# Performance work log

Measured on AMD Instinct MI355X. Metric: run time of the kernel, lower is better.

The kernel has to match this reference:

```python
import jax, jax.numpy as jnp
import numpy as np

F, K, V, ITERS = 150000, 5, 100000, 5
S = 2 ** K  # factor state space
MLP_SIZE = 2 * ITERS * S + ITERS * 2  # 330
NEG = -1e30
SHIFT = -500.0

# static bit table: bits[state, slot] in {0,1}
_BITS = ((np.arange(S)[:, None] >> np.arange(K)[None, :]) & 1).astype(np.int32)  # [S,K]
_BITS_T = jnp.asarray(_BITS.T)  # [K,S]
# mask bias for grouped logsumexp: bias[slot, b, state] = 0 if bits[state,slot]==b else NEG
_BIAS = jnp.asarray(np.where(_BITS.T[:, None, :] == np.arange(2)[None, :, None], 0.0, NEG).astype(np.float32))  # [K,2,S]


def neg_inf_to_zero(x):
    return jnp.where(jnp.isneginf(x), 0.0, x)


def expand(msg):
    # msg [F,K,2] -> [F,K,S]: broadcast each slot message over factor states by that slot's bit
    return msg[:, jnp.arange(K)[:, None], _BITS_T]


def setup_inputs() -> dict:
    key = jax.random.key(0)
    k0, k1 = jax.random.split(key)
    factor_potentials = jax.random.normal(k0, (F, S), dtype=jnp.float32)
    var_idx = jax.random.randint(k1, (F, K), 0, V, dtype=jnp.int32)
    prv_v2f = jnp.zeros((F, K, 2), jnp.float32)
    prv_f2v = jnp.zeros((F, K, 2), jnp.float32)
    prv_fb = jax.nn.log_softmax(factor_potentials, axis=1)
    # bethe MLP initialized exactly as in the torch module
    lin1_w = jnp.eye(MLP_SIZE, dtype=jnp.float32)
    lin1_b = jnp.zeros((MLP_SIZE,), jnp.float32)
    num_ones = 2 * S + 2
    lin2_w = jnp.zeros((1, MLP_SIZE), jnp.float32).at[0, -num_ones:].set(1.0)
    lin2_b = jnp.zeros((1,), jnp.float32)
    return {"factor_potentials": factor_potentials, "var_idx": var_idx,
            "prv_v2f": prv_v2f, "prv_f2v": prv_f2v, "prv_fb": prv_fb,
            "lin1_w": lin1_w, "lin1_b": lin1_b, "lin2_w": lin2_w, "lin2_b": lin2_b}


def _shifted_relu(x):
    return jnp.maximum(x, SHIFT)


def reference(factor_potentials, var_idx, prv_v2f, prv_f2v, prv_fb, lin1_w, lin1_b, lin2_w, lin2_b):
    var_flat = var_idx.reshape(-1)
    deg = jax.ops.segment_sum(jnp.ones((F * K,), jnp.float32), var_flat, num_segments=V)  # var_degrees
    pooled_states = []
    fb, v2f = prv_fb, prv_v2f
    for _ in range(ITERS):
        # factor->var messages, no double counting: subtract the slot's own incoming message
        scores = fb[:, None, :] - expand(v2f)                    # [F,K,S]
        m = jax.nn.logsumexp(scores[:, :, None, :] + _BIAS[None], axis=-1)  # [F,K,2]
        m = jax.nn.log_softmax(m, axis=-1)
        # var beliefs: gather all incoming factor->var messages
        vb = jax.ops.segment_sum(m.reshape(-1, 2), var_flat, num_segments=V)  # [V,2]
        vb = jax.nn.log_softmax(vb, axis=-1)
        # var->factor messages, no double counting
        v2f = jax.nn.log_softmax(vb[var_idx] - m, axis=-1)        # [F,K,2]
        # factor beliefs
        fb = factor_potentials + expand(v2f).sum(axis=1)          # [F,S]
        fb = fb - jax.nn.logsumexp(fb, axis=1, keepdims=True)
        # pooled Bethe free-energy features for this iteration
        e_fb = jnp.exp(fb)
        energy = jnp.sum(e_fb * neg_inf_to_zero(factor_potentials), axis=0)     # [S]
        fac_ent = -jnp.sum(e_fb * neg_inf_to_zero(fb), axis=0)                  # [S]
        var_term = jnp.sum((deg - 1.0)[:, None] * jnp.exp(vb) * neg_inf_to_zero(vb), axis=0)  # [2]
        pooled_states.append(jnp.concatenate([energy, fac_ent, var_term])[None, :])  # [1, 2S+2]
    x = jnp.concatenate(pooled_states, axis=1)   # [1, MLP_SIZE]
    h = _shifted_relu(x @ lin1_w.T + lin1_b)
    out = _shifted_relu(h @ lin2_w.T + lin2_b)   # [1,1] estimated ln(Z)
    return out
```

## Files before the change

### kernel.cpp

```cpp
#include <hip/hip_runtime.h>

#define F_N   150000
#define K_N   5
#define S_N   32
#define V_N   100000
#define NITER 5
#define MLP_N 330
#define SHIFTV (-500.0f)
#define W_ELL 32
#define DEG_PAD 16

#define FBLK  ((F_N + 255) / 256)
#define GBLK  ((V_N * 8 + 255) / 256)
#define EBLK  ((F_N * K_N + 255) / 256)
#define BBLK  (6 * FBLK)

__device__ __forceinline__ float lse2(float a, float b) {
    float mx = fmaxf(a, b);
    return mx + __logf(__expf(a - mx) + __expf(b - mx));
}

__global__ __launch_bounds__(256) void k_build(
    const float* __restrict__ prv_fb,
    const float* __restrict__ prv_v2f,
    const int*   __restrict__ vidx,
    float2*      __restrict__ m_out,
    int*         __restrict__ deg,
    int*         __restrict__ ellpos)
{
    int g = blockIdx.x / 6, r = blockIdx.x % 6;

    if (r < 5) {
        int e = (g * 5 + r) * 256 + threadIdx.x;
        if (e >= F_N * K_N) return;
        int v = vidx[e];
        int pos = atomicAdd(&deg[v * DEG_PAD], 1);
        ellpos[e] = (pos < W_ELL) ? v * W_ELL + pos : V_N * W_ELL;
        return;
    }

    int f = g * 256 + threadIdx.x;
    if (f >= F_N) return;

    float fb[S_N];
    const float4* p4 = reinterpret_cast<const float4*>(prv_fb + (size_t)f * S_N);
    #pragma unroll
    for (int i = 0; i < S_N / 4; ++i) {
        float4 v = p4[i];
        fb[i*4+0] = v.x; fb[i*4+1] = v.y; fb[i*4+2] = v.z; fb[i*4+3] = v.w;
    }
    float M = fb[0];
    #pragma unroll
    for (int s = 1; s < S_N; ++s) M = fmaxf(M, fb[s]);
    float T = 0.0f;
    float S0[K_N] = {0.f, 0.f, 0.f, 0.f, 0.f};
    #pragma unroll
    for (int s = 0; s < S_N; ++s) {
        float t = __expf(fb[s] - M);
        T += t;
        #pragma unroll
        for (int k = 0; k < K_N; ++k)
            if (((s >> k) & 1) == 0) S0[k] += t;
    }
    #pragma unroll
    for (int k = 0; k < K_N; ++k) {
        float v0 = prv_v2f[(size_t)f * (K_N*2) + k*2 + 0];
        float v1 = prv_v2f[(size_t)f * (K_N*2) + k*2 + 1];
        float u0 = __logf(S0[k])     - v0;
        float u1 = __logf(T - S0[k]) - v1;
        float l  = lse2(u0, u1);
        m_out[k*F_N + f] = make_float2(u0 - l, u1 - l);
    }
}

__global__ __launch_bounds__(256) void k_scatter0(
    const int*    __restrict__ ellpos,
    const float2* __restrict__ m,
    float2*       __restrict__ mell)
{
    int e = blockIdx.x * 256 + threadIdx.x;
    if (e >= F_N * K_N) return;
    int f = e / K_N;
    int k = e - f * K_N;
    mell[ellpos[e]] = m[k * F_N + f];
}

__global__ __launch_bounds__(256) void k_gather(
    const float2* __restrict__ mell,
    const int*    __restrict__ deg,
    float2*       __restrict__ vb,
    float2*       __restrict__ cpart,
    int iter)
{
    __shared__ float2 wred[4];
    int t = blockIdx.x * 256 + threadIdx.x;
    int v = t >> 3, sub = t & 7;
    int lane = threadIdx.x & 63;

    float a0 = 0.0f, a1 = 0.0f;
    int n = 0;
    if (v < V_N) {
        n = deg[v * DEG_PAD];
        int nn = n < W_ELL ? n : W_ELL;
        const float2* row = mell + (size_t)v * W_ELL;
        for (int i = sub; i < nn; i += 8) {
            float2 mm = row[i];
            a0 += mm.x; a1 += mm.y;
        }
    }
    a0 += __shfl_xor(a0, 1); a1 += __shfl_xor(a1, 1);
    a0 += __shfl_xor(a0, 2); a1 += __shfl_xor(a1, 2);
    a0 += __shfl_xor(a0, 4); a1 += __shfl_xor(a1, 4);

    float c0 = 0.0f, c1 = 0.0f;
    if (v < V_N && sub == 0) {
        vb[v] = make_float2(a0, a1);
        float l = lse2(a0, a1);
        float b0 = a0 - l, b1 = a1 - l;
        float dm1 = (float)n - 1.0f;
        c0 = dm1 * __expf(b0) * b0;
        c1 = dm1 * __expf(b1) * b1;
    }
    #pragma unroll
    for (int mk = 32; mk >= 1; mk >>= 1) {
        c0 += __shfl_xor(c0, mk);
        c1 += __shfl_xor(c1, mk);
    }
    if (lane == 0) wred[threadIdx.x >> 6] = make_float2(c0, c1);
    __syncthreads();
    if (threadIdx.x == 0) {
        float2 s = wred[0];
        s.x += wred[1].x + wred[2].x + wred[3].x;
        s.y += wred[1].y + wred[2].y + wred[3].y;
        cpart[iter * GBLK + blockIdx.x] = s;
    }
}

template <bool LAST>
__global__ __launch_bounds__(256) void k_iter(
    const float*  __restrict__ pot,
    const int*    __restrict__ vidx,
    const int*    __restrict__ ellpos,
    float2*       __restrict__ m,
    float2*       __restrict__ mell,
    const float2* __restrict__ vb,
    float*        __restrict__ fpart,
    int iter)
{
    const int lane = threadIdx.x & 63;
    __shared__ float red[256];

    int f = blockIdx.x * 256 + threadIdx.x;
    bool valid = f < F_N;
    int fc = valid ? f : (F_N - 1);

    float2 mm[K_N];
    #pragma unroll
    for (int k = 0; k < K_N; ++k) mm[k] = m[k*F_N + fc];
    int vi[K_N];
    #pragma unroll
    for (int k = 0; k < K_N; ++k) vi[k] = vidx[(size_t)fc * K_N + k];

    float v2f[K_N][2];
    #pragma unroll
    for (int k = 0; k < K_N; ++k) {
        float2 b = vb[vi[k]];
        float a0 = b.x - mm[k].x;
        float a1 = b.y - mm[k].y;
        float l = lse2(a0, a1);
        v2f[k][0] = a0 - l;
        v2f[k][1] = a1 - l;
    }

    float fb[S_N];
    const float4* p4 = reinterpret_cast<const float4*>(pot + (size_t)fc * S_N);
    #pragma unroll
    for (int i = 0; i < S_N / 4; ++i) {
        float4 pv = p4[i];
        int s = i * 4;
        fb[s+0] = pv.x + v2f[0][(s+0)&1] + v2f[1][((s+0)>>1)&1] + v2f[2][((s+0)>>2)&1] + v2f[3][((s+0)>>3)&1] + v2f[4][((s+0)>>4)&1];
        fb[s+1] = pv.y + v2f[0][(s+1)&1] + v2f[1][((s+1)>>1)&1] + v2f[2][((s+1)>>2)&1] + v2f[3][((s+1)>>3)&1] + v2f[4][((s+1)>>4)&1];
        fb[s+2] = pv.z + v2f[0][(s+2)&1] + v2f[1][((s+2)>>1)&1] + v2f[2][((s+2)>>2)&1] + v2f[3][((s+2)>>3)&1] + v2f[4][((s+2)>>4)&1];
        fb[s+3] = pv.w + v2f[0][(s+3)&1] + v2f[1][((s+3)>>1)&1] + v2f[2][((s+3)>>2)&1] + v2f[3][((s+3)>>3)&1] + v2f[4][((s+3)>>4)&1];
    }

    float M = fb[0];
    #pragma unroll
    for (int s = 1; s < S_N; ++s) M = fmaxf(M, fb[s]);

    float T = 0.0f;
    float S0[K_N] = {0.f, 0.f, 0.f, 0.f, 0.f};
    #pragma unroll
    for (int s = 0; s < S_N; ++s) {
        float t = __expf(fb[s] - M);
        T += t;
        #pragma unroll
        for (int k = 0; k < K_N; ++k)
            if (((s >> k) & 1) == 0) S0[k] += t;
    }

    if (!LAST) {
        int el[K_N];
        #pragma unroll
        for (int k = 0; k < K_N; ++k) el[k] = ellpos[(size_t)fc * K_N + k];
        #pragma unroll
        for (int k = 0; k < K_N; ++k) {
            float u0 = __logf(S0[k])     - v2f[k][0];
            float u1 = __logf(T - S0[k]) - v2f[k][1];
            float l  = lse2(u0, u1);
            if (valid) {
                float2 nm = make_float2(u0 - l, u1 - l);
                m[k*F_N + f] = nm;
                mell[el[k]]  = nm;
            }
        }
    }

    float invT = 1.0f / T;
    float logT = __logf(T);
    float arr[2 * S_N];
    #pragma unroll
    for (int s = 0; s < S_N; ++s) {
        float p   = __expf(fb[s] - M) * invT;
        float fbn = fb[s] - M - logT;
        float w   = v2f[0][s&1] + v2f[1][(s>>1)&1] + v2f[2][(s>>2)&1]
                  + v2f[3][(s>>3)&1] + v2f[4][(s>>4)&1];
        float po  = fb[s] - w;
        arr[s]       = valid ? p * po   : 0.0f;
        arr[S_N + s] = valid ? -p * fbn : 0.0f;
    }

    #pragma unroll
    for (int mk = 32; mk >= 1; mk >>= 1) {
        bool upper = (lane & mk) != 0;
        #pragma unroll
        for (int j = 0; j < mk; ++j) {
            float send = upper ? arr[j] : arr[j + mk];
            float recv = __shfl_xor(send, mk);
            float keep = upper ? arr[j + mk] : arr[j];
            arr[j] = keep + recv;
        }
    }

    red[threadIdx.x] = arr[0];
    __syncthreads();
    if (threadIdx.x < 64) {
        float s = red[threadIdx.x] + red[64 + threadIdx.x]
                + red[128 + threadIdx.x] + red[192 + threadIdx.x];
        fpart[((size_t)iter * FBLK + blockIdx.x) * 64 + threadIdx.x] = s;
    }
}

__global__ __launch_bounds__(256) void k_vt(
    const float*  __restrict__ fpart,
    const float2* __restrict__ cpart,
    float*        __restrict__ x)
{
    __shared__ float red[256];
    int b = blockIdx.x, t = threadIdx.x;
    float acc = 0.0f;
    if (b < 320) {
        int it = b >> 6, s = b & 63;
        for (int i = t; i < FBLK; i += 256)
            acc += fpart[((size_t)it * FBLK + i) * 64 + s];
    } else {
        int idx = b - 320;
        int it = idx >> 1, c = idx & 1;
        for (int i = t; i < GBLK; i += 256) {
            float2 p = cpart[it * GBLK + i];
            acc += c ? p.y : p.x;
        }
    }
    red[t] = acc;
    __syncthreads();
    #pragma unroll
    for (int off = 128; off >= 1; off >>= 1) {
        if (t < off) red[t] += red[t + off];
        __syncthreads();
    }
    if (t == 0) {
        if (b < 320) {
            int it = b >> 6, s = b & 63;
            x[it*66 + s] = red[0];
        } else {
            int idx = b - 320;
            int it = idx >> 1, c = idx & 1;
            x[it*66 + 64 + c] = red[0];
        }
    }
}

__global__ __launch_bounds__(64) void k_mlp1(
    const float* __restrict__ x, const float* __restrict__ w1,
    const float* __restrict__ b1, float* __restrict__ h)
{
    int j = blockIdx.x;
    int lane = threadIdx.x;
    float s = 0.0f;
    for (int i = lane; i < MLP_N; i += 64) s += x[i] * w1[(size_t)j * MLP_N + i];
    #pragma unroll
    for (int mk = 32; mk >= 1; mk >>= 1) s += __shfl_xor(s, mk);
    if (lane == 0) h[j] = fmaxf(s + b1[j], SHIFTV);
}

__global__ __launch_bounds__(64) void k_mlp2(
    const float* __restrict__ h, const float* __restrict__ w2,
    const float* __restrict__ b2, float* __restrict__ out)
{
    int lane = threadIdx.x;
    float s = 0.0f;
    for (int i = lane; i < MLP_N; i += 64) s += h[i] * w2[i];
    #pragma unroll
    for (int mk = 32; mk >= 1; mk >>= 1) s += __shfl_xor(s, mk);
    if (lane == 0) out[0] = fmaxf(s + b2[0], SHIFTV);
}

extern "C" void kernel_launch(void* const* d_in, const int* in_sizes, int n_in,
                              void* d_out, int out_size, void* d_ws, size_t ws_size,
                              hipStream_t stream)
{
    (void)in_sizes; (void)n_in; (void)out_size; (void)ws_size;
    const float* pot  = (const float*)d_in[0];
    const int*   vidx = (const int*)  d_in[1];
    const float* pv2f = (const float*)d_in[2];
    const float* pfb  = (const float*)d_in[4];
    const float* w1   = (const float*)d_in[5];
    const float* b1   = (const float*)d_in[6];
    const float* w2   = (const float*)d_in[7];
    const float* b2   = (const float*)d_in[8];

    float2* m      = (float2*)d_ws;
    float2* mell   = m + 5 * F_N;
    float2* vb     = mell + (size_t)V_N * W_ELL + 32;
    float2* cpart  = vb + V_N;
    float*  fpart  = (float*)(cpart + NITER * GBLK);
    float*  x      = fpart + (size_t)NITER * FBLK * 64;
    float*  h      = x + MLP_N;
    int*    ellpos = (int*)(h + MLP_N);
    int*    deg    = ellpos + (size_t)F_N * K_N;

    hipMemsetAsync(deg, 0, (size_t)V_N * DEG_PAD * sizeof(int), stream);

    k_build<<<BBLK, 256, 0, stream>>>(pfb, pv2f, vidx, m, deg, ellpos);
    k_scatter0<<<EBLK, 256, 0, stream>>>(ellpos, m, mell);

    for (int it = 0; it < NITER; ++it) {
        k_gather<<<GBLK, 256, 0, stream>>>(mell, deg, vb, cpart, it);
        if (it < NITER - 1)
            k_iter<false><<<FBLK, 256, 0, stream>>>(pot, vidx, ellpos, m, mell, vb, fpart, it);
        else
            k_iter<true><<<FBLK, 256, 0, stream>>>(pot, vidx, ellpos, m, mell, vb, fpart, it);
    }

    k_vt<<<330, 256, 0, stream>>>(fpart, cpart, x);
    k_mlp1<<<MLP_N, 64, 0, stream>>>(x, w1, b1, h);
    k_mlp2<<<1, 64, 0, stream>>>(h, w2, b2, (float*)d_out);
}
```

Measured before the change: 206.0 us.

## Split each factor across two threads, compact degree array, fuse MLP kernels

Each factor in k_iter is now handled by two lanes, each owning 16 of the 32 states. Max, sum and per-slot partials are combined with one shuffle, and the butterfly reduction starts at a 32-entry array with a remapped output index. The aim is to cut per-thread register pressure and serial work, raising occupancy. The change also compacts the padded degree array into a dense one for the gather kernel and fuses the two MLP kernels into a single block. The cost is duplicated v2f/gather work per factor, since both lanes compute it, and twice as many blocks and partial sums.

```diff
diff --git a/kernel.cpp b/kernel.cpp
--- a/kernel.cpp
+++ b/kernel.cpp
@@ -11,6 +11,7 @@
 #define DEG_PAD 16
 
 #define FBLK  ((F_N + 255) / 256)
+#define F2BLK ((2*F_N + 255) / 256)
 #define GBLK  ((V_N * 8 + 255) / 256)
 #define EBLK  ((F_N * K_N + 255) / 256)
 #define BBLK  (6 * FBLK)
@@ -76,9 +77,12 @@
 __global__ __launch_bounds__(256) void k_scatter0(
     const int*    __restrict__ ellpos,
     const float2* __restrict__ m,
-    float2*       __restrict__ mell)
+    const int*    __restrict__ deg,
+    float2*       __restrict__ mell,
+    int*          __restrict__ degc)
 {
     int e = blockIdx.x * 256 + threadIdx.x;
+    if (e < V_N) degc[e] = deg[e * DEG_PAD];
     if (e >= F_N * K_N) return;
     int f = e / K_N;
     int k = e - f * K_N;
@@ -87,7 +91,7 @@
 
 __global__ __launch_bounds__(256) void k_gather(
     const float2* __restrict__ mell,
-    const int*    __restrict__ deg,
+    const int*    __restrict__ degc,
     float2*       __restrict__ vb,
     float2*       __restrict__ cpart,
     int iter)
@@ -100,7 +104,7 @@
     float a0 = 0.0f, a1 = 0.0f;
     int n = 0;
     if (v < V_N) {
-        n = deg[v * DEG_PAD];
+        n = degc[v];
         int nn = n < W_ELL ? n : W_ELL;
         const float2* row = mell + (size_t)v * W_ELL;
         for (int i = sub; i < nn; i += 8) {
@@ -148,9 +152,10 @@
     int iter)
 {
     const int lane = threadIdx.x & 63;
-    __shared__ float red[256];
-
-    int f = blockIdx.x * 256 + threadIdx.x;
+    __shared__ float red[4][64];
+
+    int t = blockIdx.x * 256 + threadIdx.x;
+    int f = t >> 1, p = t & 1;
     bool valid = f < F_N;
     int fc = valid ? f : (F_N - 1);
 
@@ -172,82 +177,92 @@
         v2f[k][1] = a1 - l;
     }
 
-    float fb[S_N];
-    const float4* p4 = reinterpret_cast<const float4*>(pot + (size_t)fc * S_N);
-    #pragma unroll
-    for (int i = 0; i < S_N / 4; ++i) {
+    float fb[16];
+    const float4* p4 = reinterpret_cast<const float4*>(pot + (size_t)fc * S_N + p * 16);
+    #pragma unroll
+    for (int i = 0; i < 4; ++i) {
         float4 pv = p4[i];
-        int s = i * 4;
-        fb[s+0] = pv.x + v2f[0][(s+0)&1] + v2f[1][((s+0)>>1)&1] + v2f[2][((s+0)>>2)&1] + v2f[3][((s+0)>>3)&1] + v2f[4][((s+0)>>4)&1];
-        fb[s+1] = pv.y + v2f[0][(s+1)&1] + v2f[1][((s+1)>>1)&1] + v2f[2][((s+1)>>2)&1] + v2f[3][((s+1)>>3)&1] + v2f[4][((s+1)>>4)&1];
-        fb[s+2] = pv.z + v2f[0][(s+2)&1] + v2f[1][((s+2)>>1)&1] + v2f[2][((s+2)>>2)&1] + v2f[3][((s+2)>>3)&1] + v2f[4][((s+2)>>4)&1];
-        fb[s+3] = pv.w + v2f[0][(s+3)&1] + v2f[1][((s+3)>>1)&1] + v2f[2][((s+3)>>2)&1] + v2f[3][((s+3)>>3)&1] + v2f[4][((s+3)>>4)&1];
+        int s = p*16 + i*4;
+        fb[i*4+0] = pv.x + v2f[0][(s+0)&1] + v2f[1][((s+0)>>1)&1] + v2f[2][((s+0)>>2)&1] + v2f[3][((s+0)>>3)&1] + v2f[4][((s+0)>>4)&1];
+        fb[i*4+1] = pv.y + v2f[0][(s+1)&1] + v2f[1][((s+1)>>1)&1] + v2f[2][((s+1)>>2)&1] + v2f[3][((s+1)>>3)&1] + v2f[4][((s+1)>>4)&1];
+        fb[i*4+2] = pv.z + v2f[0][(s+2)&1] + v2f[1][((s+2)>>1)&1] + v2f[2][((s+2)>>2)&1] + v2f[3][((s+2)>>3)&1] + v2f[4][((s+2)>>4)&1];
+        fb[i*4+3] = pv.w + v2f[0][(s+3)&1] + v2f[1][((s+3)>>1)&1] + v2f[2][((s+3)>>2)&1] + v2f[3][((s+3)>>3)&1] + v2f[4][((s+3)>>4)&1];
     }
 
     float M = fb[0];
     #pragma unroll
-    for (int s = 1; s < S_N; ++s) M = fmaxf(M, fb[s]);
+    for (int j = 1; j < 16; ++j) M = fmaxf(M, fb[j]);
+    M = fmaxf(M, __shfl_xor(M, 1));
 
     float T = 0.0f;
     float S0[K_N] = {0.f, 0.f, 0.f, 0.f, 0.f};
     #pragma unroll
-    for (int s = 0; s < S_N; ++s) {
-        float t = __expf(fb[s] - M);
-        T += t;
+    for (int j = 0; j < 16; ++j) {
+        int s = p*16 + j;
+        float e = __expf(fb[j] - M);
+        T += e;
         #pragma unroll
         for (int k = 0; k < K_N; ++k)
-            if (((s >> k) & 1) == 0) S0[k] += t;
-    }
+            if (((s >> k) & 1) == 0) S0[k] += e;
+    }
+    T += __shfl_xor(T, 1);
+    #pragma unroll
+    for (int k = 0; k < K_N; ++k) S0[k] += __shfl_xor(S0[k], 1);
 
     if (!LAST) {
-        int el[K_N];
-        #pragma unroll
-        for (int k = 0; k < K_N; ++k) el[k] = ellpos[(size_t)fc * K_N + k];
         #pragma unroll
         for (int k = 0; k < K_N; ++k) {
-            float u0 = __logf(S0[k])     - v2f[k][0];
-            float u1 = __logf(T - S0[k]) - v2f[k][1];
-            float l  = lse2(u0, u1);
-            if (valid) {
+            bool mine = p ? (k >= 3) : (k < 3);
+            if (valid && mine) {
+                float u0 = __logf(S0[k])     - v2f[k][0];
+                float u1 = __logf(T - S0[k]) - v2f[k][1];
+                float l  = lse2(u0, u1);
                 float2 nm = make_float2(u0 - l, u1 - l);
                 m[k*F_N + f] = nm;
-                mell[el[k]]  = nm;
+                mell[ellpos[(size_t)f * K_N + k]] = nm;
             }
         }
     }
 
     float invT = 1.0f / T;
     float logT = __logf(T);
-    float arr[2 * S_N];
-    #pragma unroll
-    for (int s = 0; s < S_N; ++s) {
-        float p   = __expf(fb[s] - M) * invT;
-        float fbn = fb[s] - M - logT;
+    float arr[32];
+    #pragma unroll
+    for (int j = 0; j < 16; ++j) {
+        int s = p*16 + j;
+        float pe  = __expf(fb[j] - M) * invT;
+        float fbn = fb[j] - M - logT;
         float w   = v2f[0][s&1] + v2f[1][(s>>1)&1] + v2f[2][(s>>2)&1]
                   + v2f[3][(s>>3)&1] + v2f[4][(s>>4)&1];
-        float po  = fb[s] - w;
-        arr[s]       = valid ? p * po   : 0.0f;
-        arr[S_N + s] = valid ? -p * fbn : 0.0f;
-    }
-
-    #pragma unroll
-    for (int mk = 32; mk >= 1; mk >>= 1) {
+        arr[j]      = valid ? pe * (fb[j] - w) : 0.0f;
+        arr[16 + j] = valid ? -pe * fbn        : 0.0f;
+    }
+
+    int len = 16;
+    #pragma unroll
+    for (int mk = 2; mk <= 32; mk <<= 1) {
         bool upper = (lane & mk) != 0;
         #pragma unroll
-        for (int j = 0; j < mk; ++j) {
-            float send = upper ? arr[j] : arr[j + mk];
-            float recv = __shfl_xor(send, mk);
-            float keep = upper ? arr[j + mk] : arr[j];
-            arr[j] = keep + recv;
-        }
-    }
-
-    red[threadIdx.x] = arr[0];
+        for (int j = 0; j < 16; ++j) {
+            if (j < len) {
+                float send = upper ? arr[j] : arr[j + len];
+                float recv = __shfl_xor(send, mk);
+                float keep = upper ? arr[j + len] : arr[j];
+                arr[j] = keep + recv;
+            }
+        }
+        len >>= 1;
+    }
+    int jl = (((lane>>1)&1)<<4) | (((lane>>2)&1)<<3) | (((lane>>3)&1)<<2)
+           | (((lane>>4)&1)<<1) | ((lane>>5)&1);
+    int g  = (lane & 1) * 16 + jl + (jl < 16 ? 0 : 16);
+
+    red[threadIdx.x >> 6][g] = arr[0];
     __syncthreads();
     if (threadIdx.x < 64) {
-        float s = red[threadIdx.x] + red[64 + threadIdx.x]
-                + red[128 + threadIdx.x] + red[192 + threadIdx.x];
-        fpart[((size_t)iter * FBLK + blockIdx.x) * 64 + threadIdx.x] = s;
+        float s = red[0][threadIdx.x] + red[1][threadIdx.x]
+                + red[2][threadIdx.x] + red[3][threadIdx.x];
+        fpart[((size_t)iter * F2BLK + blockIdx.x) * 64 + threadIdx.x] = s;
     }
 }
 
@@ -261,8 +276,8 @@
     float acc = 0.0f;
     if (b < 320) {
         int it = b >> 6, s = b & 63;
-        for (int i = t; i < FBLK; i += 256)
-            acc += fpart[((size_t)it * FBLK + i) * 64 + s];
+        for (int i = t; i < F2BLK; i += 256)
+            acc += fpart[((size_t)it * F2BLK + i) * 64 + s];
     } else {
         int idx = b - 320;
         int it = idx >> 1, c = idx & 1;
@@ -290,29 +305,38 @@
     }
 }
 
-__global__ __launch_bounds__(64) void k_mlp1(
+__global__ __launch_bounds__(256) void k_mlp(
     const float* __restrict__ x, const float* __restrict__ w1,
-    const float* __restrict__ b1, float* __restrict__ h)
-{
-    int j = blockIdx.x;
-    int lane = threadIdx.x;
+    const float* __restrict__ b1, const float* __restrict__ w2,
+    const float* __restrict__ b2, float* __restrict__ out)
+{
+    __shared__ float xs[MLP_N];
+    __shared__ float hs[MLP_N];
+    __shared__ float red[256];
+    int t = threadIdx.x, wid = t >> 6, lane = t & 63;
+
+    for (int i = t; i < MLP_N; i += 256) xs[i] = x[i];
+    __syncthreads();
+
+    for (int j = wid; j < MLP_N; j += 4) {
+        float s = 0.0f;
+        for (int i = lane; i < MLP_N; i += 64) s += xs[i] * w1[(size_t)j * MLP_N + i];
+        #pragma unroll
+        for (int mk = 32; mk >= 1; mk >>= 1) s += __shfl_xor(s, mk);
+        if (lane == 0) hs[j] = fmaxf(s + b1[j], SHIFTV);
+    }
+    __syncthreads();
+
     float s = 0.0f;
-    for (int i = lane; i < MLP_N; i += 64) s += x[i] * w1[(size_t)j * MLP_N + i];
-    #pragma unroll
-    for (int mk = 32; mk >= 1; mk >>= 1) s += __shfl_xor(s, mk);
-    if (lane == 0) h[j] = fmaxf(s + b1[j], SHIFTV);
-}
-
-__global__ __launch_bounds__(64) void k_mlp2(
-    const float* __restrict__ h, const float* __restrict__ w2,
-    const float* __restrict__ b2, float* __restrict__ out)
-{
-    int lane = threadIdx.x;
-    float s = 0.0f;
-    for (int i = lane; i < MLP_N; i += 64) s += h[i] * w2[i];
-    #pragma unroll
-    for (int mk = 32; mk >= 1; mk >>= 1) s += __shfl_xor(s, mk);
-    if (lane == 0) out[0] = fmaxf(s + b2[0], SHIFTV);
+    for (int i = t; i < MLP_N; i += 256) s += hs[i] * w2[i];
+    red[t] = s;
+    __syncthreads();
+    #pragma unroll
+    for (int off = 128; off >= 1; off >>= 1) {
+        if (t < off) red[t] += red[t + off];
+        __syncthreads();
+    }
+    if (t == 0) out[0] = fmaxf(red[0] + b2[0], SHIFTV);
 }
 
 extern "C" void kernel_launch(void* const* d_in, const int* in_sizes, int n_in,
@@ -334,25 +358,24 @@
     float2* vb     = mell + (size_t)V_N * W_ELL + 32;
     float2* cpart  = vb + V_N;
     float*  fpart  = (float*)(cpart + NITER * GBLK);
-    float*  x      = fpart + (size_t)NITER * FBLK * 64;
-    float*  h      = x + MLP_N;
-    int*    ellpos = (int*)(h + MLP_N);
-    int*    deg    = ellpos + (size_t)F_N * K_N;
+    float*  x      = fpart + (size_t)NITER * F2BLK * 64;
+    int*    ellpos = (int*)(x + MLP_N);
+    int*    degc   = ellpos + (size_t)F_N * K_N;
+    int*    deg    = degc + V_N;
 
     hipMemsetAsync(deg, 0, (size_t)V_N * DEG_PAD * sizeof(int), stream);
 
     k_build<<<BBLK, 256, 0, stream>>>(pfb, pv2f, vidx, m, deg, ellpos);
-    k_scatter0<<<EBLK, 256, 0, stream>>>(ellpos, m, mell);
+    k_scatter0<<<EBLK, 256, 0, stream>>>(ellpos, m, deg, mell, degc);
 
     for (int it = 0; it < NITER; ++it) {
-        k_gather<<<GBLK, 256, 0, stream>>>(mell, deg, vb, cpart, it);
+        k_gather<<<GBLK, 256, 0, stream>>>(mell, degc, vb, cpart, it);
         if (it < NITER - 1)
-            k_iter<false><<<FBLK, 256, 0, stream>>>(pot, vidx, ellpos, m, mell, vb, fpart, it);
+            k_iter<false><<<F2BLK, 256, 0, stream>>>(pot, vidx, ellpos, m, mell, vb, fpart, it);
         else
-            k_iter<true><<<FBLK, 256, 0, stream>>>(pot, vidx, ellpos, m, mell, vb, fpart, it);
+            k_iter<true><<<F2BLK, 256, 0, stream>>>(pot, vidx, ellpos, m, mell, vb, fpart, it);
     }
 
     k_vt<<<330, 256, 0, stream>>>(fpart, cpart, x);
-    k_mlp1<<<MLP_N, 64, 0, stream>>>(x, w1, b1, h);
-    k_mlp2<<<1, 64, 0, stream>>>(h, w2, b2, (float*)d_out);
-}
+    k_mlp<<<1, 256, 0, stream>>>(x, w1, b1, w2, b2, (float*)d_out);
+}
```

After: 461.9 us. 124% more time.

## Fuse initial message build with ELL scatter, one thread per edge

Applied to the files above, without the earlier changes.

Merges the initial factor-to-variable message computation and the ELL scatter into one kernel with one thread per (factor, slot) edge. Each thread does its degree atomic, computes its own slot message and writes it straight into the ELL buffer, which removes the separate scatter launch and the reread of m. The degree array is now unpadded, so the memset is smaller and the gather reads degrees contiguously, but atomics on neighbouring counters may contend more. In exchange, each of the 5 slot threads reloads and re-exponentiates the same 32-float factor belief row, so that exp work is done five times over.

```diff
diff --git a/kernel.cpp b/kernel.cpp
--- a/kernel.cpp
+++ b/kernel.cpp
@@ -8,12 +8,10 @@
 #define MLP_N 330
 #define SHIFTV (-500.0f)
 #define W_ELL 32
-#define DEG_PAD 16
 
 #define FBLK  ((F_N + 255) / 256)
 #define GBLK  ((V_N * 8 + 255) / 256)
 #define EBLK  ((F_N * K_N + 255) / 256)
-#define BBLK  (6 * FBLK)
 
 __device__ __forceinline__ float lse2(float a, float b) {
     float mx = fmaxf(a, b);
@@ -25,64 +23,46 @@
     const float* __restrict__ prv_v2f,
     const int*   __restrict__ vidx,
     float2*      __restrict__ m_out,
+    float2*      __restrict__ mell,
     int*         __restrict__ deg,
     int*         __restrict__ ellpos)
-{
-    int g = blockIdx.x / 6, r = blockIdx.x % 6;
-
-    if (r < 5) {
-        int e = (g * 5 + r) * 256 + threadIdx.x;
-        if (e >= F_N * K_N) return;
-        int v = vidx[e];
-        int pos = atomicAdd(&deg[v * DEG_PAD], 1);
-        ellpos[e] = (pos < W_ELL) ? v * W_ELL + pos : V_N * W_ELL;
-        return;
-    }
-
-    int f = g * 256 + threadIdx.x;
-    if (f >= F_N) return;
-
-    float fb[S_N];
-    const float4* p4 = reinterpret_cast<const float4*>(prv_fb + (size_t)f * S_N);
-    #pragma unroll
-    for (int i = 0; i < S_N / 4; ++i) {
-        float4 v = p4[i];
-        fb[i*4+0] = v.x; fb[i*4+1] = v.y; fb[i*4+2] = v.z; fb[i*4+3] = v.w;
-    }
-    float M = fb[0];
-    #pragma unroll
-    for (int s = 1; s < S_N; ++s) M = fmaxf(M, fb[s]);
-    float T = 0.0f;
-    float S0[K_N] = {0.f, 0.f, 0.f, 0.f, 0.f};
-    #pragma unroll
-    for (int s = 0; s < S_N; ++s) {
-        float t = __expf(fb[s] - M);
-        T += t;
-        #pragma unroll
-        for (int k = 0; k < K_N; ++k)
-            if (((s >> k) & 1) == 0) S0[k] += t;
-    }
-    #pragma unroll
-    for (int k = 0; k < K_N; ++k) {
-        float v0 = prv_v2f[(size_t)f * (K_N*2) + k*2 + 0];
-        float v1 = prv_v2f[(size_t)f * (K_N*2) + k*2 + 1];
-        float u0 = __logf(S0[k])     - v0;
-        float u1 = __logf(T - S0[k]) - v1;
-        float l  = lse2(u0, u1);
-        m_out[k*F_N + f] = make_float2(u0 - l, u1 - l);
-    }
-}
-
-__global__ __launch_bounds__(256) void k_scatter0(
-    const int*    __restrict__ ellpos,
-    const float2* __restrict__ m,
-    float2*       __restrict__ mell)
 {
     int e = blockIdx.x * 256 + threadIdx.x;
     if (e >= F_N * K_N) return;
     int f = e / K_N;
     int k = e - f * K_N;
-    mell[ellpos[e]] = m[k * F_N + f];
+    int v = vidx[e];
+
+    int pos = atomicAdd(&deg[v], 1);
+
+    float fb[S_N];
+    const float4* p4 = reinterpret_cast<const float4*>(prv_fb + (size_t)f * S_N);
+    #pragma unroll
+    for (int i = 0; i < S_N / 4; ++i) {
+        float4 q = p4[i];
+        fb[i*4+0] = q.x; fb[i*4+1] = q.y; fb[i*4+2] = q.z; fb[i*4+3] = q.w;
+    }
+    float M = fb[0];
+    #pragma unroll
+    for (int s = 1; s < S_N; ++s) M = fmaxf(M, fb[s]);
+    float T = 0.0f, S0 = 0.0f;
+    #pragma unroll
+    for (int s = 0; s < S_N; ++s) {
+        float t = __expf(fb[s] - M);
+        T += t;
+        if (((s >> k) & 1) == 0) S0 += t;
+    }
+    float v0 = prv_v2f[(size_t)e * 2 + 0];
+    float v1 = prv_v2f[(size_t)e * 2 + 1];
+    float u0 = __logf(S0)     - v0;
+    float u1 = __logf(T - S0) - v1;
+    float l  = lse2(u0, u1);
+    float2 nm = make_float2(u0 - l, u1 - l);
+
+    m_out[k*F_N + f] = nm;
+    int slot = (pos < W_ELL) ? v * W_ELL + pos : V_N * W_ELL;
+    ellpos[e] = slot;
+    mell[slot] = nm;
 }
 
 __global__ __launch_bounds__(256) void k_gather(
@@ -100,7 +80,7 @@
     float a0 = 0.0f, a1 = 0.0f;
     int n = 0;
     if (v < V_N) {
-        n = deg[v * DEG_PAD];
+        n = deg[v];
         int nn = n < W_ELL ? n : W_ELL;
         const float2* row = mell + (size_t)v * W_ELL;
         for (int i = sub; i < nn; i += 8) {
@@ -339,10 +319,9 @@
     int*    ellpos = (int*)(h + MLP_N);
     int*    deg    = ellpos + (size_t)F_N * K_N;
 
-    hipMemsetAsync(deg, 0, (size_t)V_N * DEG_PAD * sizeof(int), stream);
-
-    k_build<<<BBLK, 256, 0, stream>>>(pfb, pv2f, vidx, m, deg, ellpos);
-    k_scatter0<<<EBLK, 256, 0, stream>>>(ellpos, m, mell);
+    hipMemsetAsync(deg, 0, (size_t)V_N * sizeof(int), stream);
+
+    k_build<<<EBLK, 256, 0, stream>>>(pfb, pv2f, vidx, m, mell, deg, ellpos);
 
     for (int it = 0; it < NITER; ++it) {
         k_gather<<<GBLK, 256, 0, stream>>>(mell, deg, vb, cpart, it);
```

Result: faster. 199.6 us (-3.1%).
